# Optimization experiments

Measured on AMD Instinct MI355X. Metric: run time of the kernel, lower is better.

Reference implementation:

```python
import jax, jax.numpy as jnp
import numpy as np
import math

B, NQ, NK, D = 8, 2048, 2048, 512
EPS = 1e-8


def setup_inputs() -> dict:
    key = jax.random.key(0)
    k1, k2, k3 = jax.random.split(key, 3)
    qs = jax.random.normal(k1, (B, NQ, D), dtype=jnp.float32)
    ks = jax.random.normal(k2, (B, NK, D), dtype=jnp.float32)
    vs = jax.random.normal(k3, (B, NK, D), dtype=jnp.float32)
    scale = jnp.full((1,), math.sqrt(D), dtype=jnp.float32)  # nn.Parameter(sqrt(dim))
    bias = jnp.zeros((), dtype=jnp.float32)
    return {"qs": qs, "ks": ks, "vs": vs, "scale": scale, "bias": bias}


def _lorentz_self_inner(u):
    # <u,u>_L = -u0^2 + sum_{i>0} u_i^2 = sum u_i^2 - 2*u0^2, keepdim on last axis
    return jnp.sum(u * u, axis=-1, keepdims=True) - 2.0 * (u[..., :1] ** 2)


def reference(qs, ks, vs, scale, bias):
    # cinner: Minkowski inner product, time coord (index 0) sign-flipped on qs
    q_flip = qs.at[..., 0].multiply(-1.0)
    att = -jnp.einsum('bqd,bkd->bqk', q_flip, ks)  # -cinner(qs, ks)
    att = jax.nn.softmax(att / scale + bias, axis=-1)
    # Einstein/Lorentz midpoint: weighted sum then renormalize to the hyperboloid (k=1)
    ave = jnp.einsum('bqk,bkd->bqd', att, vs)
    denom = jnp.sqrt(jnp.clip(jnp.abs(-_lorentz_self_inner(ave)), EPS, None))
    return ave / denom
```

## Files before the change

kernel.cpp:

```cpp
#include <hip/hip_runtime.h>

#define NSEQ 2048
#define DIM  512
#define NKT  64
#define TILEB 32768
#define SHIFT 12.0f
#define SMEMB (4 * TILEB + 4096)

typedef __bf16 bf16x8 __attribute__((ext_vector_type(8)));
typedef float  f32x4  __attribute__((ext_vector_type(4)));

__device__ __forceinline__ void gld16(const void* g, void* l) {
  __builtin_amdgcn_global_load_lds(
      (const __attribute__((address_space(1))) unsigned int*)g,
      (__attribute__((address_space(3))) unsigned int*)l, 16, 0, 0);
}

#define MFMA __builtin_amdgcn_mfma_f32_16x16x32_bf16

__global__ __launch_bounds__(256) void prep_kv(const float* __restrict__ ks,
                                               const float* __restrict__ vs,
                                               char* __restrict__ kp,
                                               char* __restrict__ vtp) {
  __shared__ __align__(16) char lds[TILEB];
  int id = blockIdx.x;
  int t = threadIdx.x;
  if (id < 512) {
    int b = id >> 6, kt = id & 63;
    const float* src = ks + ((size_t)(b * NSEQ + kt * 32)) * DIM;
    char* dst = kp + ((size_t)(b * 64 + kt)) * TILEB;
#pragma unroll
    for (int i = 0; i < 8; ++i) {
      int c = t + i * 256;
      int row = c >> 6;
      int d0 = (c & 63) * 8;
      const float4* s4 = (const float4*)(src + row * DIM + d0);
      float4 x = s4[0], y = s4[1];
      bf16x8 h;
      h[0] = (__bf16)x.x; h[1] = (__bf16)x.y; h[2] = (__bf16)x.z; h[3] = (__bf16)x.w;
      h[4] = (__bf16)y.x; h[5] = (__bf16)y.y; h[6] = (__bf16)y.z; h[7] = (__bf16)y.w;
      *(bf16x8*)(dst + row * 1024 + ((d0 * 2) ^ ((row & 7) << 4))) = h;
    }
  } else {
    int v = id - 512;
    int b = v >> 6, kt = v & 63;
    const float* src = vs + ((size_t)(b * NSEQ + kt * 32)) * DIM;
#pragma unroll
    for (int i = 0; i < 8; ++i) {
      int c = t + i * 256;
      int kv = c >> 6;
      int d0 = (c & 63) * 8;
      const float4* s4 = (const float4*)(src + kv * DIM + d0);
      float4 x = s4[0], y = s4[1];
      float vals[8] = {x.x, x.y, x.z, x.w, y.x, y.y, y.z, y.w};
#pragma unroll
      for (int jj = 0; jj < 8; ++jj) {
        int d = d0 + jj;
        int byte = (d >> 1) * 128 + (((((d & 1) * 64) + kv * 2)) ^ (((d >> 1) & 7) << 4));
        *(__bf16*)(lds + byte) = (__bf16)vals[jj];
      }
    }
    __syncthreads();
    char* dst = vtp + ((size_t)(b * 64 + kt)) * TILEB;
#pragma unroll
    for (int i = 0; i < 8; ++i) {
      int c16 = t + i * 256;
      *(bf16x8*)(dst + c16 * 16) = *(const bf16x8*)(lds + c16 * 16);
    }
  }
}

__global__ __launch_bounds__(256) void attn_main(
    const float* __restrict__ qs, const char* __restrict__ kp,
    const char* __restrict__ vtp, const float* __restrict__ scale,
    float* __restrict__ out) {
  extern __shared__ __align__(16) char smem[];
  int b  = blockIdx.x & 7;
  int qt = blockIdx.x >> 3;
  int tid = threadIdx.x;
  int w = tid >> 6, lane = tid & 63;
  int c = lane & 15, g = lane >> 4;
  int q0 = qt * 64 + w * 16;

  char* kbuf = smem;
  char* vbuf = smem + 2 * TILEB;
  char* plds = smem + 4 * TILEB + w * 1024;

  float cc = 1.4426950408889634f / scale[0];

  bf16x8 qf[16];
#pragma unroll
  for (int k = 0; k < 16; ++k) {
    int d = k * 32 + g * 8;
    const float4* p = (const float4*)(qs + ((size_t)(b * NSEQ + q0 + c)) * DIM + d);
    float4 x = p[0], y = p[1];
    float vals[8] = {x.x, x.y, x.z, x.w, y.x, y.y, y.z, y.w};
    bf16x8 hh;
#pragma unroll
    for (int jj = 0; jj < 8; ++jj) {
      float mlt = (d + jj == 0) ? cc : -cc;
      hh[jj] = (__bf16)(vals[jj] * mlt);
    }
    qf[k] = hh;
  }

  f32x4 acc[32];
#pragma unroll
  for (int i = 0; i < 32; ++i) acc[i] = (f32x4){0.f, 0.f, 0.f, 0.f};

  const char* kpb = kp  + (size_t)b * 64 * TILEB;
  const char* vpb = vtp + (size_t)b * 64 * TILEB;

  const int csw = (c & 7) << 4;
  const int vt_lane = (c >> 1) * 128 +
      (((((c & 1) * 64) + g * 16)) ^ (((c >> 1) & 7) << 4));
  const int qb = (c >> 1) * 128;
  const int qh = (c & 1) * 64;
  const int qx = ((c >> 1) & 7) << 4;

#pragma unroll
  for (int i = 0; i < 8; ++i) {
    int o = tid * 16 + i * 4096;
    gld16(kpb + o, kbuf + o);
    gld16(vpb + o, vbuf + o);
    gld16(kpb + TILEB + o, kbuf + TILEB + o);
  }
  __syncthreads();

  bf16x8 pf;

  {
    f32x4 sa0 = {0,0,0,0}, sb0 = {0,0,0,0}, sa1 = {0,0,0,0}, sb1 = {0,0,0,0};
    const char* krl = kbuf + c * 1024;
    const char* krh = krl + 16 * 1024;
#pragma unroll
    for (int k = 0; k < 16; ++k) {
      int bir = (k * 64 + g * 16) ^ csw;
      bf16x8 kfl = *(const bf16x8*)(krl + bir);
      bf16x8 kfh = *(const bf16x8*)(krh + bir);
      if (k & 1) { sb0 = MFMA(kfl, qf[k], sb0, 0,0,0); sb1 = MFMA(kfh, qf[k], sb1, 0,0,0); }
      else       { sa0 = MFMA(kfl, qf[k], sa0, 0,0,0); sa1 = MFMA(kfh, qf[k], sa1, 0,0,0); }
    }
    f32x4 sl = sa0 + sb0, sh = sa1 + sb1;
#pragma unroll
    for (int r = 0; r < 4; ++r) {
      float pvl = exp2f(sl[r] - SHIFT);
      float pvh = exp2f(sh[r] - SHIFT);
      int kvl = 4 * g + r;
      *(__bf16*)(plds + qb + ((qh + kvl * 2) ^ qx))        = (__bf16)pvl;
      *(__bf16*)(plds + qb + ((qh + (16 + kvl) * 2) ^ qx)) = (__bf16)pvh;
    }
    pf = *(const bf16x8*)(plds + vt_lane);
  }
  __syncthreads();

  for (int t = 0; t < NKT - 1; ++t) {
    if (t + 2 < NKT) {
      const char* ksrc = kpb + (size_t)(t + 2) * TILEB;
      char* kdst = kbuf + (t & 1) * TILEB;
#pragma unroll
      for (int i = 0; i < 8; ++i) {
        int o = tid * 16 + i * 4096;
        gld16(ksrc + o, kdst + o);
      }
    }
    {
      const char* vsrc = vpb + (size_t)(t + 1) * TILEB;
      char* vdst = vbuf + ((t + 1) & 1) * TILEB;
#pragma unroll
      for (int i = 0; i < 8; ++i) {
        int o = tid * 16 + i * 4096;
        gld16(vsrc + o, vdst + o);
      }
    }

    f32x4 sa0 = {0,0,0,0}, sb0 = {0,0,0,0}, sa1 = {0,0,0,0}, sb1 = {0,0,0,0};
    const char* krl = kbuf + ((t + 1) & 1) * TILEB + c * 1024;
    const char* krh = krl + 16 * 1024;
    const char* vr  = vbuf + (t & 1) * TILEB + vt_lane;
#pragma unroll
    for (int k = 0; k < 16; ++k) {
      int bir = (k * 64 + g * 16) ^ csw;
      bf16x8 kfl = *(const bf16x8*)(krl + bir);
      bf16x8 kfh = *(const bf16x8*)(krh + bir);
      bf16x8 vf0 = *(const bf16x8*)(vr + (2 * k) * 1024);
      bf16x8 vf1 = *(const bf16x8*)(vr + (2 * k + 1) * 1024);
      if (k & 1) { sb0 = MFMA(kfl, qf[k], sb0, 0,0,0); sb1 = MFMA(kfh, qf[k], sb1, 0,0,0); }
      else       { sa0 = MFMA(kfl, qf[k], sa0, 0,0,0); sa1 = MFMA(kfh, qf[k], sa1, 0,0,0); }
      acc[2 * k]     = MFMA(pf, vf0, acc[2 * k], 0, 0, 0);
      acc[2 * k + 1] = MFMA(pf, vf1, acc[2 * k + 1], 0, 0, 0);
    }
    f32x4 sl = sa0 + sb0, sh = sa1 + sb1;

#pragma unroll
    for (int r = 0; r < 4; ++r) {
      float pvl = exp2f(sl[r] - SHIFT);
      float pvh = exp2f(sh[r] - SHIFT);
      int kvl = 4 * g + r;
      *(__bf16*)(plds + qb + ((qh + kvl * 2) ^ qx))        = (__bf16)pvl;
      *(__bf16*)(plds + qb + ((qh + (16 + kvl) * 2) ^ qx)) = (__bf16)pvh;
    }
    pf = *(const bf16x8*)(plds + vt_lane);

    __syncthreads();
  }

  {
    const char* vr = vbuf + ((NKT - 1) & 1) * TILEB + vt_lane;
#pragma unroll
    for (int dtl = 0; dtl < 32; ++dtl) {
      bf16x8 vf = *(const bf16x8*)(vr + dtl * 1024);
      acc[dtl] = MFMA(pf, vf, acc[dtl], 0, 0, 0);
    }
  }

#pragma unroll
  for (int r = 0; r < 4; ++r) {
    float ss = 0.f;
#pragma unroll
    for (int dtl = 0; dtl < 32; ++dtl) ss += acc[dtl][r] * acc[dtl][r];
    ss += __shfl_xor(ss, 1);
    ss += __shfl_xor(ss, 2);
    ss += __shfl_xor(ss, 4);
    ss += __shfl_xor(ss, 8);
    float a0 = __shfl(acc[0][r], lane & 48);
    float d2 = fabsf(2.f * a0 * a0 - ss);
    float inv = rsqrtf(fmaxf(d2, 1e-8f));
    float* orow = out + ((size_t)(b * NSEQ + q0 + 4 * g + r)) * DIM + c;
#pragma unroll
    for (int dtl = 0; dtl < 32; ++dtl) orow[dtl * 16] = acc[dtl][r] * inv;
  }
}

extern "C" void kernel_launch(void* const* d_in, const int* in_sizes, int n_in,
                              void* d_out, int out_size, void* d_ws, size_t ws_size,
                              hipStream_t stream) {
  (void)in_sizes; (void)n_in; (void)out_size;
  const float* qs = (const float*)d_in[0];
  const float* ks = (const float*)d_in[1];
  const float* vs = (const float*)d_in[2];
  const float* scale = (const float*)d_in[3];
  float* out = (float*)d_out;

  size_t need = (size_t)2 * 8 * 64 * TILEB;
  if (ws_size < need) return;
  char* kp  = (char*)d_ws;
  char* vtp = (char*)d_ws + (size_t)8 * 64 * TILEB;

  hipFuncSetAttribute((const void*)attn_main,
                      hipFuncAttributeMaxDynamicSharedMemorySize, SMEMB);

  prep_kv<<<1024, 256, 0, stream>>>(ks, vs, kp, vtp);
  attn_main<<<256, 256, SMEMB, stream>>>(qs, kp, vtp, scale, out);
}
```

Baseline: 139.7 us.

## Split D across wave pairs, each wave handles two query groups

Adds a new attention kernel in which four waves form a 2x2 grid: two query halves of 32 rows and two D halves of 256. Each wave computes QK^T for 32 queries, which doubles reuse of each K fragment load, and runs PV only on its own half of D. The kernel needs an LDS exchange of partial squared norms to normalise the output. Occupancy is pinned to one wave per EU, and a runtime check falls back to the old kernel if the new one spills to scratch. In exchange QK^T work is duplicated across the two D-half waves, register pressure rises, and the host adds an attribute query on every launch.

```diff
diff --git a/kernel.cpp b/kernel.cpp
--- a/kernel.cpp
+++ b/kernel.cpp
@@ -5,7 +5,8 @@
 #define NKT  64
 #define TILEB 32768
 #define SHIFT 12.0f
-#define SMEMB (4 * TILEB + 4096)
+#define SMEMB_DS (4 * TILEB + 8192)
+#define SMEMB_FB (4 * TILEB + 4096)
 
 typedef __bf16 bf16x8 __attribute__((ext_vector_type(8)));
 typedef float  f32x4  __attribute__((ext_vector_type(4)));
@@ -70,7 +71,239 @@
   }
 }
 
-__global__ __launch_bounds__(256) void attn_main(
+__global__
+__attribute__((amdgpu_flat_work_group_size(256, 256)))
+__attribute__((amdgpu_waves_per_eu(1, 1)))
+void attn_ds(const float* __restrict__ qs, const char* __restrict__ kp,
+             const char* __restrict__ vtp, const float* __restrict__ scale,
+             float* __restrict__ out) {
+  extern __shared__ __align__(16) char smem[];
+  int b  = blockIdx.x & 7;
+  int qt = blockIdx.x >> 3;
+  int tid = threadIdx.x;
+  int w = tid >> 6, lane = tid & 63;
+  int wq = w & 1, wd = w >> 1;
+  int c = lane & 15, g = lane >> 4;
+  int q0 = qt * 64 + wq * 32;
+
+  char* kbuf = smem;
+  char* vbuf = smem + 2 * TILEB;
+  char* pldsA = smem + 4 * TILEB + w * 2048;
+  char* pldsB = pldsA + 1024;
+
+  float cc = 1.4426950408889634f / scale[0];
+
+  bf16x8 qfA[16], qfB[16];
+#pragma unroll
+  for (int k = 0; k < 16; ++k) {
+    int d = k * 32 + g * 8;
+#pragma unroll
+    for (int grp = 0; grp < 2; ++grp) {
+      int row = q0 + grp * 16 + c;
+      const float4* p = (const float4*)(qs + ((size_t)(b * NSEQ + row)) * DIM + d);
+      float4 x = p[0], y = p[1];
+      float vals[8] = {x.x, x.y, x.z, x.w, y.x, y.y, y.z, y.w};
+      bf16x8 hh;
+#pragma unroll
+      for (int jj = 0; jj < 8; ++jj) {
+        float mlt = (d + jj == 0) ? cc : -cc;
+        hh[jj] = (__bf16)(vals[jj] * mlt);
+      }
+      if (grp == 0) qfA[k] = hh; else qfB[k] = hh;
+    }
+  }
+
+  f32x4 accA[16], accB[16];
+#pragma unroll
+  for (int i = 0; i < 16; ++i) { accA[i] = (f32x4){0,0,0,0}; accB[i] = (f32x4){0,0,0,0}; }
+
+  const char* kpb = kp  + (size_t)b * 64 * TILEB;
+  const char* vpb = vtp + (size_t)b * 64 * TILEB;
+
+  const int csw = (c & 7) << 4;
+  const int vt_lane = (c >> 1) * 128 +
+      (((((c & 1) * 64) + g * 16)) ^ (((c >> 1) & 7) << 4));
+  const int qb = (c >> 1) * 128;
+  const int qh = (c & 1) * 64;
+  const int qx = ((c >> 1) & 7) << 4;
+
+#pragma unroll
+  for (int i = 0; i < 8; ++i) {
+    int o = tid * 16 + i * 4096;
+    gld16(kpb + o, kbuf + o);
+    gld16(vpb + o, vbuf + o);
+    gld16(kpb + TILEB + o, kbuf + TILEB + o);
+  }
+  __syncthreads();
+
+  bf16x8 pfA, pfB;
+
+  {
+    f32x4 aA0={0,0,0,0}, bA0={0,0,0,0}, aA1={0,0,0,0}, bA1={0,0,0,0};
+    f32x4 aB0={0,0,0,0}, bB0={0,0,0,0}, aB1={0,0,0,0}, bB1={0,0,0,0};
+    const char* krl = kbuf + c * 1024;
+    const char* krh = krl + 16384;
+#pragma unroll
+    for (int k = 0; k < 16; ++k) {
+      int bir = (k * 64 + g * 16) ^ csw;
+      bf16x8 kfl = *(const bf16x8*)(krl + bir);
+      bf16x8 kfh = *(const bf16x8*)(krh + bir);
+      if (k & 1) {
+        bA0 = MFMA(kfl, qfA[k], bA0,0,0,0); bA1 = MFMA(kfh, qfA[k], bA1,0,0,0);
+        bB0 = MFMA(kfl, qfB[k], bB0,0,0,0); bB1 = MFMA(kfh, qfB[k], bB1,0,0,0);
+      } else {
+        aA0 = MFMA(kfl, qfA[k], aA0,0,0,0); aA1 = MFMA(kfh, qfA[k], aA1,0,0,0);
+        aB0 = MFMA(kfl, qfB[k], aB0,0,0,0); aB1 = MFMA(kfh, qfB[k], aB1,0,0,0);
+      }
+    }
+    f32x4 slA = aA0 + bA0, shA = aA1 + bA1;
+    f32x4 slB = aB0 + bB0, shB = aB1 + bB1;
+#pragma unroll
+    for (int r = 0; r < 4; ++r) {
+      int kvl = 4 * g + r;
+      *(__bf16*)(pldsA + qb + ((qh + kvl * 2) ^ qx))        = (__bf16)exp2f(slA[r] - SHIFT);
+      *(__bf16*)(pldsA + qb + ((qh + (16 + kvl) * 2) ^ qx)) = (__bf16)exp2f(shA[r] - SHIFT);
+      *(__bf16*)(pldsB + qb + ((qh + kvl * 2) ^ qx))        = (__bf16)exp2f(slB[r] - SHIFT);
+      *(__bf16*)(pldsB + qb + ((qh + (16 + kvl) * 2) ^ qx)) = (__bf16)exp2f(shB[r] - SHIFT);
+    }
+    pfA = *(const bf16x8*)(pldsA + vt_lane);
+    pfB = *(const bf16x8*)(pldsB + vt_lane);
+  }
+  __syncthreads();
+
+  for (int t = 0; t < NKT - 1; ++t) {
+    if (t + 2 < NKT) {
+      const char* ksrc = kpb + (size_t)(t + 2) * TILEB;
+      char* kdst = kbuf + (t & 1) * TILEB;
+#pragma unroll
+      for (int i = 0; i < 8; ++i) {
+        int o = tid * 16 + i * 4096;
+        gld16(ksrc + o, kdst + o);
+      }
+    }
+    {
+      const char* vsrc = vpb + (size_t)(t + 1) * TILEB;
+      char* vdst = vbuf + ((t + 1) & 1) * TILEB;
+#pragma unroll
+      for (int i = 0; i < 8; ++i) {
+        int o = tid * 16 + i * 4096;
+        gld16(vsrc + o, vdst + o);
+      }
+    }
+
+    f32x4 aA0={0,0,0,0}, bA0={0,0,0,0}, aA1={0,0,0,0}, bA1={0,0,0,0};
+    f32x4 aB0={0,0,0,0}, bB0={0,0,0,0}, aB1={0,0,0,0}, bB1={0,0,0,0};
+    const char* krl = kbuf + ((t + 1) & 1) * TILEB + c * 1024;
+    const char* krh = krl + 16384;
+    const char* vr  = vbuf + (t & 1) * TILEB + wd * 16384 + vt_lane;
+#pragma unroll
+    for (int k = 0; k < 16; ++k) {
+      int bir = (k * 64 + g * 16) ^ csw;
+      bf16x8 kfl = *(const bf16x8*)(krl + bir);
+      bf16x8 kfh = *(const bf16x8*)(krh + bir);
+      bf16x8 vf  = *(const bf16x8*)(vr + k * 1024);
+      if (k & 1) {
+        bA0 = MFMA(kfl, qfA[k], bA0,0,0,0); bA1 = MFMA(kfh, qfA[k], bA1,0,0,0);
+        bB0 = MFMA(kfl, qfB[k], bB0,0,0,0); bB1 = MFMA(kfh, qfB[k], bB1,0,0,0);
+      } else {
+        aA0 = MFMA(kfl, qfA[k], aA0,0,0,0); aA1 = MFMA(kfh, qfA[k], aA1,0,0,0);
+        aB0 = MFMA(kfl, qfB[k], aB0,0,0,0); aB1 = MFMA(kfh, qfB[k], aB1,0,0,0);
+      }
+      accA[k] = MFMA(pfA, vf, accA[k], 0, 0, 0);
+      accB[k] = MFMA(pfB, vf, accB[k], 0, 0, 0);
+    }
+    f32x4 slA = aA0 + bA0, shA = aA1 + bA1;
+    f32x4 slB = aB0 + bB0, shB = aB1 + bB1;
+
+#pragma unroll
+    for (int r = 0; r < 4; ++r) {
+      int kvl = 4 * g + r;
+      *(__bf16*)(pldsA + qb + ((qh + kvl * 2) ^ qx))        = (__bf16)exp2f(slA[r] - SHIFT);
+      *(__bf16*)(pldsA + qb + ((qh + (16 + kvl) * 2) ^ qx)) = (__bf16)exp2f(shA[r] - SHIFT);
+      *(__bf16*)(pldsB + qb + ((qh + kvl * 2) ^ qx))        = (__bf16)exp2f(slB[r] - SHIFT);
+      *(__bf16*)(pldsB + qb + ((qh + (16 + kvl) * 2) ^ qx)) = (__bf16)exp2f(shB[r] - SHIFT);
+    }
+    pfA = *(const bf16x8*)(pldsA + vt_lane);
+    pfB = *(const bf16x8*)(pldsB + vt_lane);
+
+    __syncthreads();
+  }
+
+  {
+    const char* vr = vbuf + ((NKT - 1) & 1) * TILEB + wd * 16384 + vt_lane;
+#pragma unroll
+    for (int dtl = 0; dtl < 16; ++dtl) {
+      bf16x8 vf = *(const bf16x8*)(vr + dtl * 1024);
+      accA[dtl] = MFMA(pfA, vf, accA[dtl], 0, 0, 0);
+      accB[dtl] = MFMA(pfB, vf, accB[dtl], 0, 0, 0);
+    }
+  }
+  __syncthreads();
+
+  float* ex = (float*)smem;
+  float ssA[4], ssB[4];
+#pragma unroll
+  for (int r = 0; r < 4; ++r) {
+    float sA = 0.f, sB = 0.f;
+#pragma unroll
+    for (int dtl = 0; dtl < 16; ++dtl) {
+      sA += accA[dtl][r] * accA[dtl][r];
+      sB += accB[dtl][r] * accB[dtl][r];
+    }
+    sA += __shfl_xor(sA, 1); sA += __shfl_xor(sA, 2);
+    sA += __shfl_xor(sA, 4); sA += __shfl_xor(sA, 8);
+    sB += __shfl_xor(sB, 1); sB += __shfl_xor(sB, 2);
+    sB += __shfl_xor(sB, 4); sB += __shfl_xor(sB, 8);
+    ssA[r] = sA; ssB[r] = sB;
+  }
+  if (wd == 1 && c == 0) {
+#pragma unroll
+    for (int r = 0; r < 4; ++r) {
+      ex[wq * 32 + 4 * g + r]      = ssA[r];
+      ex[wq * 32 + 16 + 4 * g + r] = ssB[r];
+    }
+  }
+  __syncthreads();
+  if (wd == 0) {
+#pragma unroll
+    for (int r = 0; r < 4; ++r) {
+      float sfA = ssA[r] + ex[wq * 32 + 4 * g + r];
+      float sfB = ssB[r] + ex[wq * 32 + 16 + 4 * g + r];
+      float a0A = __shfl(accA[0][r], lane & 48);
+      float a0B = __shfl(accB[0][r], lane & 48);
+      float invA = rsqrtf(fmaxf(fabsf(2.f * a0A * a0A - sfA), 1e-8f));
+      float invB = rsqrtf(fmaxf(fabsf(2.f * a0B * a0B - sfB), 1e-8f));
+      if (c == 0) {
+        ex[64 + wq * 32 + 4 * g + r]      = invA;
+        ex[64 + wq * 32 + 16 + 4 * g + r] = invB;
+      }
+      float* orA = out + ((size_t)(b * NSEQ + q0 + 4 * g + r)) * DIM + c;
+      float* orB = out + ((size_t)(b * NSEQ + q0 + 16 + 4 * g + r)) * DIM + c;
+#pragma unroll
+      for (int dtl = 0; dtl < 16; ++dtl) {
+        orA[dtl * 16] = accA[dtl][r] * invA;
+        orB[dtl * 16] = accB[dtl][r] * invB;
+      }
+    }
+  }
+  __syncthreads();
+  if (wd == 1) {
+#pragma unroll
+    for (int r = 0; r < 4; ++r) {
+      float invA = ex[64 + wq * 32 + 4 * g + r];
+      float invB = ex[64 + wq * 32 + 16 + 4 * g + r];
+      float* orA = out + ((size_t)(b * NSEQ + q0 + 4 * g + r)) * DIM + 256 + c;
+      float* orB = out + ((size_t)(b * NSEQ + q0 + 16 + 4 * g + r)) * DIM + 256 + c;
+#pragma unroll
+      for (int dtl = 0; dtl < 16; ++dtl) {
+        orA[dtl * 16] = accA[dtl][r] * invA;
+        orB[dtl * 16] = accB[dtl][r] * invB;
+      }
+    }
+  }
+}
+
+__global__ __launch_bounds__(256) void attn_fb(
     const float* __restrict__ qs, const char* __restrict__ kp,
     const char* __restrict__ vtp, const float* __restrict__ scale,
     float* __restrict__ out) {
@@ -128,7 +361,6 @@
   __syncthreads();
 
   bf16x8 pf;
-
   {
     f32x4 sa0 = {0,0,0,0}, sb0 = {0,0,0,0}, sa1 = {0,0,0,0}, sb1 = {0,0,0,0};
     const char* krl = kbuf + c * 1024;
@@ -144,11 +376,9 @@
     f32x4 sl = sa0 + sb0, sh = sa1 + sb1;
 #pragma unroll
     for (int r = 0; r < 4; ++r) {
-      float pvl = exp2f(sl[r] - SHIFT);
-      float pvh = exp2f(sh[r] - SHIFT);
       int kvl = 4 * g + r;
-      *(__bf16*)(plds + qb + ((qh + kvl * 2) ^ qx))        = (__bf16)pvl;
-      *(__bf16*)(plds + qb + ((qh + (16 + kvl) * 2) ^ qx)) = (__bf16)pvh;
+      *(__bf16*)(plds + qb + ((qh + kvl * 2) ^ qx))        = (__bf16)exp2f(sl[r] - SHIFT);
+      *(__bf16*)(plds + qb + ((qh + (16 + kvl) * 2) ^ qx)) = (__bf16)exp2f(sh[r] - SHIFT);
     }
     pf = *(const bf16x8*)(plds + vt_lane);
   }
@@ -173,7 +403,6 @@
         gld16(vsrc + o, vdst + o);
       }
     }
-
     f32x4 sa0 = {0,0,0,0}, sb0 = {0,0,0,0}, sa1 = {0,0,0,0}, sb1 = {0,0,0,0};
     const char* krl = kbuf + ((t + 1) & 1) * TILEB + c * 1024;
     const char* krh = krl + 16 * 1024;
@@ -191,20 +420,15 @@
       acc[2 * k + 1] = MFMA(pf, vf1, acc[2 * k + 1], 0, 0, 0);
     }
     f32x4 sl = sa0 + sb0, sh = sa1 + sb1;
-
-#pragma unroll
-    for (int r = 0; r < 4; ++r) {
-      float pvl = exp2f(sl[r] - SHIFT);
-      float pvh = exp2f(sh[r] - SHIFT);
+#pragma unroll
+    for (int r = 0; r < 4; ++r) {
       int kvl = 4 * g + r;
-      *(__bf16*)(plds + qb + ((qh + kvl * 2) ^ qx))        = (__bf16)pvl;
-      *(__bf16*)(plds + qb + ((qh + (16 + kvl) * 2) ^ qx)) = (__bf16)pvh;
+      *(__bf16*)(plds + qb + ((qh + kvl * 2) ^ qx))        = (__bf16)exp2f(sl[r] - SHIFT);
+      *(__bf16*)(plds + qb + ((qh + (16 + kvl) * 2) ^ qx)) = (__bf16)exp2f(sh[r] - SHIFT);
     }
     pf = *(const bf16x8*)(plds + vt_lane);
-
     __syncthreads();
   }
-
   {
     const char* vr = vbuf + ((NKT - 1) & 1) * TILEB + vt_lane;
 #pragma unroll
@@ -213,7 +437,6 @@
       acc[dtl] = MFMA(pf, vf, acc[dtl], 0, 0, 0);
     }
   }
-
 #pragma unroll
   for (int r = 0; r < 4; ++r) {
     float ss = 0.f;
@@ -247,9 +470,20 @@
   char* kp  = (char*)d_ws;
   char* vtp = (char*)d_ws + (size_t)8 * 64 * TILEB;
 
-  hipFuncSetAttribute((const void*)attn_main,
-                      hipFuncAttributeMaxDynamicSharedMemorySize, SMEMB);
-
   prep_kv<<<1024, 256, 0, stream>>>(ks, vs, kp, vtp);
-  attn_main<<<256, 256, SMEMB, stream>>>(qs, kp, vtp, scale, out);
+
+  hipFuncAttributes a;
+  bool useDS = false;
+  if (hipFuncGetAttributes(&a, (const void*)attn_ds) == hipSuccess)
+    useDS = (a.localSizeBytes == 0);
+
+  if (useDS) {
+    hipFuncSetAttribute((const void*)attn_ds,
+                        hipFuncAttributeMaxDynamicSharedMemorySize, SMEMB_DS);
+    attn_ds<<<256, 256, SMEMB_DS, stream>>>(qs, kp, vtp, scale, out);
+  } else {
+    hipFuncSetAttribute((const void*)attn_fb,
+                        hipFuncAttributeMaxDynamicSharedMemorySize, SMEMB_FB);
+    attn_fb<<<256, 256, SMEMB_FB, stream>>>(qs, kp, vtp, scale, out);
+  }
 }
```

After: 172.6 us. +23.5%, slower.
